# Kernel optimization log

Measured on AMD Instinct MI355X. Metric: run time of the kernel, lower is better.

The kernel has to match this reference:

```python
import jax, jax.numpy as jnp
import numpy as np
import math

N, E, G, D, H, L = 10000, 160000, 64, 480, 4, 6
DH = D // H          # 120 dims per head
NB = 128             # number of radial basis functions
SH = 9               # 1+3+5 spherical-harmonic channels (l=0,1,2)
CUTOFF = 5.0
AVG_DEG = 15.57930850982666
AVG_NODES = 18.03065905448718


def _silu(x):
    return x * jax.nn.sigmoid(x)


def _sph_harm(vec):
    # component-normalized real spherical harmonics l=0,1,2 on unit vectors
    r = jnp.linalg.norm(vec, axis=-1, keepdims=True) + 1e-12
    u = vec / r
    x, y, z = u[:, 0], u[:, 1], u[:, 2]
    s3, s5, s15 = math.sqrt(3.0), math.sqrt(5.0), math.sqrt(15.0)
    return jnp.stack([
        jnp.ones_like(x),
        s3 * x, s3 * y, s3 * z,
        s15 * x * y, s15 * y * z,
        0.5 * s5 * (3.0 * z * z - 1.0),
        s15 * x * z, 0.5 * s15 * (x * x - y * y)], axis=-1)


def _rbf(d):
    # Gaussian radial basis, centers on [0, cutoff]
    centers = jnp.linspace(0.0, CUTOFF, NB)
    width = CUTOFF / NB
    return jnp.exp(-jnp.square((d[:, None] - centers[None, :]) / width))


def _ln(x):
    mu = jnp.mean(x, axis=-1, keepdims=True)
    var = jnp.var(x, axis=-1, keepdims=True)
    return (x - mu) * jax.lax.rsqrt(var + 1e-5)


def setup_inputs() -> dict:
    key = jax.random.key(0)
    ks = jax.random.split(key, 24)

    def w(k, shape, fan_in):
        return jax.random.normal(k, shape, jnp.float32) / math.sqrt(fan_in)

    inp = {}
    inp["pos"] = jax.random.uniform(ks[0], (N, 3), jnp.float32) * 10.0
    inp["node_atom"] = jax.random.randint(ks[1], (N,), 0, 64)
    inp["edge_src"] = jax.random.randint(ks[2], (E,), 0, N)
    inp["edge_dst"] = jax.random.randint(ks[3], (E,), 0, N)
    inp["batch"] = jnp.sort(jax.random.randint(ks[4], (N,), 0, G))
    # learned parameters
    inp["atom_table"] = w(ks[5], (64, D), 1)
    inp["Wdeg"] = w(ks[6], (SH, D), SH)
    inp["Wd1"] = w(ks[7], (NB, 64), NB)
    inp["Wd2"] = w(ks[8], (64, 64), 64)
    inp["Wd3"] = w(ks[9], (64, 1), 64)
    inp["Wq"] = w(ks[10], (L, D, D), D)
    inp["Wk"] = w(ks[11], (L, D, D), D)
    inp["Wv"] = w(ks[12], (L, D, D), D)
    inp["Wsh"] = w(ks[13], (L, SH, D), SH)
    inp["W1"] = w(ks[14], (L, NB, 64), NB)
    inp["W2"] = w(ks[15], (L, 64, 64), 64)
    inp["W3"] = w(ks[16], (L, 64, H), 64)
    inp["Wo"] = w(ks[17], (L, D, D), D)
    inp["Wf1"] = w(ks[18], (L, D, 2 * D), D)
    inp["Wf2"] = w(ks[19], (L, 2 * D, D), 2 * D)
    inp["Wh1"] = w(ks[20], (D, D), D)
    inp["Wh2"] = w(ks[21], (D, 1), D)
    return inp


def reference(pos, atom_table, Wdeg, Wd1, Wd2, Wd3, Wq, Wk, Wv, Wsh, W1, W2, W3,
              Wo, Wf1, Wf2, Wh1, Wh2, node_atom, edge_src, edge_dst, batch):
    edge_vec = pos[edge_src] - pos[edge_dst]              # [E,3]
    sh = _sph_harm(edge_vec)                              # [E,SH]
    rbf = _rbf(jnp.linalg.norm(edge_vec, axis=-1))        # [E,NB]

    # atom embedding + edge-degree embedding (scatter-sum, rescaled)
    x = atom_table[node_atom]                             # [N,D]
    g0 = _silu(_silu(rbf @ Wd1) @ Wd2) @ Wd3              # [E,1]
    deg = jax.ops.segment_sum((sh @ Wdeg) * g0, edge_dst, num_segments=N)
    x = x + deg / math.sqrt(AVG_DEG)

    inv = 1.0 / math.sqrt(DH)
    for l in range(L):
        # per-edge q/k with SH tensor-product-style mixing and RBF gate
        q = (x @ Wq[l])[edge_dst].reshape(-1, H, DH)
        k = (x[edge_src] @ Wk[l] + sh @ Wsh[l]).reshape(-1, H, DH)
        gate = _silu(_silu(rbf @ W1[l]) @ W2[l]) @ W3[l]  # [E,H]
        logits = jnp.sum(q * k, axis=-1) * inv * gate      # [E,H]
        # per-neighborhood (destination node) softmax
        m = jax.ops.segment_max(logits, edge_dst, num_segments=N)
        a = jnp.exp(logits - m[edge_dst])
        den = jax.ops.segment_sum(a, edge_dst, num_segments=N)
        alpha = a / (den[edge_dst] + 1e-12)                # [E,H]
        v = (x @ Wv[l])[edge_src].reshape(-1, H, DH)
        msg = (alpha[..., None] * v).reshape(-1, D)
        agg = jax.ops.segment_sum(msg, edge_dst, num_segments=N)
        x = _ln(x + (agg / math.sqrt(AVG_DEG)) @ Wo[l])
        x = _ln(x + _silu(x @ Wf1[l]) @ Wf2[l])

    node_e = _silu(x @ Wh1) @ Wh2                          # [N,1]
    energy = jax.ops.segment_sum(node_e[:, 0], batch, num_segments=G) / AVG_NODES
    return energy
```

## Files before the change

### kernel.cpp

```cpp
#include <hip/hip_runtime.h>
#include <hip/hip_bf16.h>

#define NN 10000
#define EE 160000
#define GG 64
#define DD 480
#define HH 4
#define LLAYERS 6
#define DHD 120
#define NB_ 128
#define TSIZE 4096
#define DMAXT 5.5f
#define LSCALE (4095.0f/5.5f)

#define INV_DH 0.09128709291752768f
#define INV_SQRT_DEG 0.25335277f
#define INV_AVG_NODES (1.0f/18.03065905448718f)

typedef __attribute__((ext_vector_type(8))) short bf16x8;
typedef __attribute__((ext_vector_type(4))) float f32x4;
typedef __attribute__((ext_vector_type(8))) unsigned short u16x8;

__device__ __forceinline__ float b2f(unsigned short u){ return __uint_as_float(((unsigned)u)<<16); }
__device__ __forceinline__ unsigned short f2b(float f){
  unsigned u = __float_as_uint(f);
  return (unsigned short)((u + 0x7fffu + ((u>>16)&1u)) >> 16);
}
__device__ __forceinline__ float wsum(float v){
  #pragma unroll
  for (int off=32; off>0; off>>=1) v += __shfl_xor(v, off, 64);
  return v;
}
__device__ __forceinline__ void glds16(const void* g, void* l) {
  __builtin_amdgcn_global_load_lds((const __attribute__((address_space(1))) unsigned int*)g,
                                   (__attribute__((address_space(3))) unsigned int*)l, 16, 0, 0);
}

__global__ __launch_bounds__(256) void zero_kernel(int* __restrict__ cnt, float* __restrict__ out){
  int i = blockIdx.x*256 + threadIdx.x;
  if (i < NN) cnt[i] = 0;
  if (i < GG) out[i] = 0.f;
}

__global__ __launch_bounds__(256) void gather_x_kernel(const float* __restrict__ at,
    const int* __restrict__ atom, float* __restrict__ x){
  const int wid = threadIdx.x >> 6, lane = threadIdx.x & 63;
  for (int n = blockIdx.x*4 + wid; n < NN; n += gridDim.x*4) {
    int a = atom[n];
    if (lane < 60) {
      const float4* src = (const float4*)(at + (size_t)a*DD + lane*8);
      float4* dst = (float4*)(x + (size_t)n*DD + lane*8);
      dst[0] = src[0]; dst[1] = src[1];
    }
  }
}

__global__ __launch_bounds__(256) void edge_geom_kernel(const float* __restrict__ pos,
    const int* __restrict__ esrc, const int* __restrict__ edst,
    float* __restrict__ sh, float* __restrict__ dedge){
  const int e = blockIdx.x*256 + threadIdx.x;
  if (e >= EE) return;
  int s = esrc[e], d = edst[e];
  float vx = pos[s*3+0]-pos[d*3+0];
  float vy = pos[s*3+1]-pos[d*3+1];
  float vz = pos[s*3+2]-pos[d*3+2];
  float rr = sqrtf(vx*vx+vy*vy+vz*vz);
  dedge[e] = rr;
  float r = rr + 1e-12f;
  float x = vx/r, y = vy/r, z = vz/r;
  const float s3 = 1.7320508075688772f;
  const float s5 = 2.23606797749979f;
  const float s15 = 3.872983346207417f;
  float* o = sh + (size_t)e*9;
  o[0] = 1.f;
  o[1] = s3*x; o[2] = s3*y; o[3] = s3*z;
  o[4] = s15*x*y; o[5] = s15*y*z;
  o[6] = 0.5f*s5*(3.f*z*z-1.f);
  o[7] = s15*x*z;
  o[8] = 0.5f*s15*(x*x-y*y);
}

__global__ __launch_bounds__(256) void hist_kernel(const int* __restrict__ edst, int* __restrict__ cnt){
  int e = blockIdx.x*256 + threadIdx.x;
  if (e < EE) atomicAdd(&cnt[edst[e]], 1);
}

__global__ __launch_bounds__(1024) void scan_kernel(const int* __restrict__ cnt,
    int* __restrict__ row_ptr, int* __restrict__ cursor){
  __shared__ int sd[1024];
  __shared__ int s_carry;
  if (threadIdx.x == 0) s_carry = 0;
  __syncthreads();
  for (int base = 0; base < NN; base += 1024) {
    int i = base + threadIdx.x;
    int v = (i < NN) ? cnt[i] : 0;
    sd[threadIdx.x] = v;
    __syncthreads();
    for (int off = 1; off < 1024; off <<= 1) {
      int t = 0;
      if ((int)threadIdx.x >= off) t = sd[threadIdx.x - off];
      __syncthreads();
      sd[threadIdx.x] += t;
      __syncthreads();
    }
    int incl = sd[threadIdx.x];
    int carry = s_carry;
    if (i < NN) { row_ptr[i] = carry + incl - v; cursor[i] = carry + incl - v; }
    __syncthreads();
    if (threadIdx.x == 1023) s_carry = carry + incl;
    __syncthreads();
  }
  if (threadIdx.x == 0) row_ptr[NN] = s_carry;
}

__global__ __launch_bounds__(256) void scatter_kernel(const int* __restrict__ esrc,
    const int* __restrict__ edst, int* __restrict__ cursor,
    int* __restrict__ eid, int* __restrict__ srcs){
  int e = blockIdx.x*256 + threadIdx.x;
  if (e < EE) {
    int n = edst[e];
    int p = atomicAdd(&cursor[n], 1);
    eid[p] = e;
    srcs[p] = esrc[e];
  }
}

__global__ __launch_bounds__(256) void table_kernel(
    const float* __restrict__ Wd1, const float* __restrict__ Wd2, const float* __restrict__ Wd3,
    const float* __restrict__ W1, const float* __restrict__ W2, const float* __restrict__ W3,
    float* __restrict__ Tg, float* __restrict__ Tl) {
  const int chain = blockIdx.y;
  const float *A1, *A2, *A3; int NC;
  if (chain == 0) { A1 = Wd1; A2 = Wd2; A3 = Wd3; NC = 1; }
  else { int l = chain-1; A1 = W1 + (size_t)l*128*64; A2 = W2 + (size_t)l*64*64; A3 = W3 + (size_t)l*64*4; NC = 4; }
  __shared__ float W1s[128*64];
  __shared__ float W2s[64*64];
  __shared__ float W3s[64*4];
  for (int i = threadIdx.x; i < 128*64; i += 256) W1s[i] = A1[i];
  for (int i = threadIdx.x; i < 64*64; i += 256) W2s[i] = A2[i];
  for (int i = threadIdx.x; i < 64*4; i += 256) W3s[i] = (i < 64*NC) ? A3[i] : 0.f;
  __syncthreads();
  const int t = blockIdx.x*256 + threadIdx.x;
  const float d = (float)t * (DMAXT/(float)(TSIZE-1));
  float t1[64];
  #pragma unroll
  for (int c = 0; c < 64; ++c) t1[c] = 0.f;
  for (int j = 0; j < 128; ++j) {
    float z = (d - (float)j*(5.0f/127.0f)) * (128.0f/5.0f);
    float f = __expf(-z*z);
    #pragma unroll
    for (int c = 0; c < 64; ++c) t1[c] += f * W1s[j*64 + c];
  }
  #pragma unroll
  for (int c = 0; c < 64; ++c) t1[c] = t1[c] / (1.f + __expf(-t1[c]));
  float t2[64];
  #pragma unroll
  for (int c = 0; c < 64; ++c) t2[c] = 0.f;
  for (int c = 0; c < 64; ++c) {
    float v = t1[c];
    #pragma unroll
    for (int c2 = 0; c2 < 64; ++c2) t2[c2] += v * W2s[c*64 + c2];
  }
  #pragma unroll
  for (int c = 0; c < 64; ++c) t2[c] = t2[c] / (1.f + __expf(-t2[c]));
  if (chain == 0) {
    float o = 0.f;
    for (int c = 0; c < 64; ++c) o += t2[c] * W3s[c];
    Tg[t] = o;
  } else {
    #pragma unroll
    for (int nc = 0; nc < 4; ++nc) {
      float o = 0.f;
      for (int c = 0; c < 64; ++c) o += t2[c] * W3s[c*4 + nc];
      Tl[((size_t)(chain-1)*TSIZE + t)*4 + nc] = o;
    }
  }
}

__device__ __forceinline__ float lookup1(const float* __restrict__ Tg, float d) {
  float u = d * LSCALE;
  if (u >= (float)(TSIZE-1)) return 0.f;
  int i = (int)u; float fr = u - (float)i;
  float a = Tg[i], b = Tg[i+1];
  return a + fr*(b-a);
}

__global__ __launch_bounds__(256) void transpose_w_kernel(const float* __restrict__ W,
    __hip_bfloat16* __restrict__ Wt, int K, int N, int Npad,
    long long lstrideW, long long lstrideT) {
  __shared__ float T[32][33];
  const int l = blockIdx.z;
  W  += (size_t)l*lstrideW;
  Wt += (size_t)l*lstrideT;
  const int k0 = blockIdx.y*32, n0 = blockIdx.x*32;
  const int tx = threadIdx.x & 31, ty = threadIdx.x >> 5;
  #pragma unroll
  for (int r = 0; r < 32; r += 8) {
    int k = k0 + ty + r, n = n0 + tx;
    T[ty+r][tx] = (k < K && n < N) ? W[(size_t)k*N + n] : 0.f;
  }
  __syncthreads();
  #pragma unroll
  for (int r = 0; r < 32; r += 8) {
    int n = n0 + ty + r, k = k0 + tx;
    if (n < Npad && k < K)
      ((unsigned short*)Wt)[(size_t)n*K + k] = f2b(T[tx][ty+r]);
  }
}

template<int SILU, int OUT>
__global__ __launch_bounds__(256) void gemm_bf16_kernel(
    const __hip_bfloat16* __restrict__ A, const __hip_bfloat16* __restrict__ Bt,
    float* __restrict__ Cf, __hip_bfloat16* __restrict__ Cb0,
    __hip_bfloat16* __restrict__ Cb1, __hip_bfloat16* __restrict__ Cb2,
    int M, int K, int Nc) {
  __shared__ char smem[(512 + 256) * 16];
  char* AsB = smem;
  char* BsB = smem + 8192;
  const int tid = threadIdx.x;
  const int lane = tid & 63, wid = tid >> 6;
  const int wm = wid >> 1, wn = wid & 1;
  const long long m0 = (long long)blockIdx.y * 128;
  const int n0 = blockIdx.x * 64;

  const int arow_loc = (wid & 1)*64 + lane;
  long long gr = m0 + arow_loc; if (gr >= M) gr = M - 1;
  const __hip_bfloat16* aptr = A + gr * (size_t)K;
  const int khiA0 = wid >> 1, khiA1 = 2 + (wid >> 1);
  char* adst0 = AsB + wid*64*16;
  char* adst1 = AsB + 4096 + wid*64*16;
  const __hip_bfloat16* bptr = Bt + (size_t)(n0 + lane) * K;
  char* bdst = BsB + wid*64*16;

  f32x4 acc[4][2];
  #pragma unroll
  for (int i = 0; i < 4; ++i)
    #pragma unroll
    for (int j = 0; j < 2; ++j)
      acc[i][j] = (f32x4){0.f,0.f,0.f,0.f};

  const int lr = lane & 15, lkh = lane >> 4;

  for (int kt = 0; kt < K; kt += 32) {
    __syncthreads();
    glds16(aptr + kt + khiA0*8, adst0);
    glds16(aptr + kt + khiA1*8, adst1);
    glds16(bptr + kt + wid*8, bdst);
    __syncthreads();
    bf16x8 afr[4], bfr[2];
    #pragma unroll
    for (int fm = 0; fm < 4; ++fm)
      afr[fm] = *reinterpret_cast<const bf16x8*>(AsB + (lkh*128 + wm*64 + fm*16 + lr)*16);
    #pragma unroll
    for (int fn = 0; fn < 2; ++fn)
      bfr[fn] = *reinterpret_cast<const bf16x8*>(BsB + (lkh*64 + wn*32 + fn*16 + lr)*16);
    #pragma unroll
    for (int fm = 0; fm < 4; ++fm)
      #pragma unroll
      for (int fn = 0; fn < 2; ++fn)
        acc[fm][fn] = __builtin_amdgcn_mfma_f32_16x16x32_bf16(afr[fm], bfr[fn], acc[fm][fn], 0, 0, 0);
  }

  const int seg = n0 >> 9;
  const int c0 = (OUT == 2) ? (n0 & 511) : n0;
  unsigned short* qdst = nullptr;
  if (OUT == 2) qdst = (unsigned short*)(seg == 0 ? Cb0 : (seg == 1 ? Cb1 : Cb2));
  #pragma unroll
  for (int fm = 0; fm < 4; ++fm) {
    #pragma unroll
    for (int fn = 0; fn < 2; ++fn) {
      #pragma unroll
      for (int j = 0; j < 4; ++j) {
        long long r = m0 + wm*64 + fm*16 + lkh*4 + j;
        int c = c0 + wn*32 + fn*16 + lr;
        if (r < M && c < Nc) {
          float v = acc[fm][fn][j];
          if (SILU) v = v / (1.f + __expf(-v));
          if (OUT == 0) Cf[r*(size_t)Nc + c] = v;
          else if (OUT == 1) ((unsigned short*)Cb0)[r*(size_t)Nc + c] = f2b(v);
          else qdst[r*(size_t)Nc + c] = f2b(v);
        }
      }
    }
  }
}

__global__ __launch_bounds__(256) void deg_kernel(const float* __restrict__ dedge,
    const float* __restrict__ sh, const float* __restrict__ Tg,
    const int* __restrict__ row_ptr, const int* __restrict__ eid,
    const float* __restrict__ Wdeg, float* __restrict__ x, __hip_bfloat16* __restrict__ xb) {
  const int wid = threadIdx.x >> 6, lane = threadIdx.x & 63;
  for (int n = blockIdx.x*4 + wid; n < NN; n += gridDim.x*4) {
    const int e0 = row_ptr[n], e1 = row_ptr[n+1];
    float s9[9] = {0,0,0,0,0,0,0,0,0};
    for (int p = e0 + lane; p < e1; p += 64) {
      int e = eid[p];
      float g = lookup1(Tg, dedge[e]);
      const float* srow = sh + (size_t)e*9;
      #pragma unroll
      for (int s = 0; s < 9; ++s) s9[s] += g*srow[s];
    }
    #pragma unroll
    for (int s = 0; s < 9; ++s) s9[s] = wsum(s9[s]);
    #pragma unroll
    for (int r = 0; r < 8; ++r) {
      int d = lane + (r<<6);
      if (d < DD) {
        float acc = 0.f;
        #pragma unroll
        for (int s = 0; s < 9; ++s) acc += s9[s]*Wdeg[s*DD + d];
        float vv = x[(size_t)n*DD + d] + acc * INV_SQRT_DEG;
        x[(size_t)n*DD + d] = vv;
        ((unsigned short*)xb)[(size_t)n*DD + d] = f2b(vv);
      }
    }
  }
}

__global__ __launch_bounds__(256) void p_kernel(const __hip_bfloat16* __restrict__ xq,
    const float* __restrict__ Wsh_l, float* __restrict__ P) {
  const int wid = threadIdx.x >> 6, lane = threadIdx.x & 63;
  for (int n = blockIdx.x*4 + wid; n < NN; n += gridDim.x*4) {
    if (lane < 36) {
      int h = lane/9, s = lane%9;
      const unsigned short* q = (const unsigned short*)(xq + (size_t)n*DD + h*DHD);
      const float* w = Wsh_l + s*DD + h*DHD;
      float acc = 0.f;
      #pragma unroll
      for (int db = 0; db < 15; ++db) {
        u16x8 v = *reinterpret_cast<const u16x8*>(q + db*8);
        #pragma unroll
        for (int j = 0; j < 8; ++j) acc += b2f(v[j])*w[db*8+j];
      }
      P[(size_t)n*36 + lane] = acc;
    }
  }
}

__global__ __launch_bounds__(256) void coef_kernel(
    const int* __restrict__ eid, const int* __restrict__ edst,
    const float* __restrict__ sh, const float* __restrict__ dedge,
    const float* __restrict__ Tl, const float* __restrict__ P,
    float2* __restrict__ sb) {
  const int p = blockIdx.x*256 + threadIdx.x;
  if (p >= EE) return;
  const int e = eid[p];
  const int n = edst[e];
  const float* srow = sh + (size_t)e*9;
  float s0 = srow[0], s1 = srow[1], s2 = srow[2], s3 = srow[3], s4 = srow[4];
  float s5 = srow[5], s6 = srow[6], s7 = srow[7], s8 = srow[8];
  const float* Pn = P + (size_t)n*36;
  float g[4];
  {
    float u = dedge[e] * LSCALE;
    if (u >= (float)(TSIZE-1)) { g[0]=g[1]=g[2]=g[3]=0.f; }
    else {
      int ti = (int)u; float fr = u - (float)ti;
      const float4 ga = *reinterpret_cast<const float4*>(Tl + ti*4);
      const float4 gb = *reinterpret_cast<const float4*>(Tl + ti*4 + 4);
      g[0] = ga.x + fr*(gb.x-ga.x); g[1] = ga.y + fr*(gb.y-ga.y);
      g[2] = ga.z + fr*(gb.z-ga.z); g[3] = ga.w + fr*(gb.w-ga.w);
    }
  }
  #pragma unroll
  for (int h = 0; h < 4; ++h) {
    const float* Ph = Pn + h*9;
    float lp = s0*Ph[0]+s1*Ph[1]+s2*Ph[2]+s3*Ph[3]+s4*Ph[4]
             + s5*Ph[5]+s6*Ph[6]+s7*Ph[7]+s8*Ph[8];
    float sc = INV_DH * g[h];
    sb[(size_t)p*4 + h] = make_float2(sc, lp*sc);
  }
}

__global__ __launch_bounds__(256) void attn_kernel(
    const __hip_bfloat16* __restrict__ xq, const __hip_bfloat16* __restrict__ xk,
    const __hip_bfloat16* __restrict__ xv, const float2* __restrict__ sb,
    const int* __restrict__ row_ptr, const int* __restrict__ srcs,
    __hip_bfloat16* __restrict__ aggout) {
  const int wid = threadIdx.x >> 6, lane = threadIdx.x & 63;
  __shared__ float l_s[4][64][4];
  __shared__ int   src_sh[4][64];
  float (*ls)[4] = l_s[wid];
  int* srcS = src_sh[wid];
  const int hh = lane >> 4, li = lane & 15;
  const int hd = (lane < 60) ? (lane/15) : 3;
  const unsigned short* xkp = (const unsigned short*)xk;
  const unsigned short* xvp = (const unsigned short*)xv;
  const int doff = hh*DHD + li*8;
  for (int n = blockIdx.x*4 + wid; n < NN; n += gridDim.x*4) {
    const int e0 = row_ptr[n], e1 = row_ptr[n+1];
    float qf[8] = {0,0,0,0,0,0,0,0};
    if (li < 15) {
      u16x8 v = *reinterpret_cast<const u16x8*>((const unsigned short*)xq + (size_t)n*DD + doff);
      #pragma unroll
      for (int j = 0; j < 8; ++j) qf[j] = b2f(v[j]);
    }
    float m_reg = -1e30f, den_reg = 0.f;
    float agg[8] = {0,0,0,0,0,0,0,0};
    for (int c0 = e0; c0 < e1; c0 += 64) {
      const int cn = min(64, e1 - c0);
      if (lane < cn) srcS[lane] = srcs[c0 + lane];
      asm volatile("s_waitcnt lgkmcnt(0)" ::: "memory");
      int i = 0;
      for (; i + 4 <= cn; i += 4) {
        int sA = srcS[i], sB = srcS[i+1], sC = srcS[i+2], sD = srcS[i+3];
        float a0 = 0.f, a1 = 0.f, a2 = 0.f, a3 = 0.f;
        if (li < 15) {
          u16x8 k0 = *reinterpret_cast<const u16x8*>(xkp + (size_t)sA*DD + doff);
          u16x8 k1 = *reinterpret_cast<const u16x8*>(xkp + (size_t)sB*DD + doff);
          u16x8 k2 = *reinterpret_cast<const u16x8*>(xkp + (size_t)sC*DD + doff);
          u16x8 k3 = *reinterpret_cast<const u16x8*>(xkp + (size_t)sD*DD + doff);
          #pragma unroll
          for (int j = 0; j < 8; ++j) {
            a0 += qf[j]*b2f(k0[j]);
            a1 += qf[j]*b2f(k1[j]);
            a2 += qf[j]*b2f(k2[j]);
            a3 += qf[j]*b2f(k3[j]);
          }
        }
        #pragma unroll
        for (int off = 1; off < 16; off <<= 1) {
          a0 += __shfl_xor(a0, off, 64);
          a1 += __shfl_xor(a1, off, 64);
          a2 += __shfl_xor(a2, off, 64);
          a3 += __shfl_xor(a3, off, 64);
        }
        if (li == 0) {
          float2 cA = sb[(size_t)(c0+i+0)*4 + hh];
          float2 cB = sb[(size_t)(c0+i+1)*4 + hh];
          float2 cC = sb[(size_t)(c0+i+2)*4 + hh];
          float2 cD = sb[(size_t)(c0+i+3)*4 + hh];
          ls[i+0][hh] = a0*cA.x + cA.y;
          ls[i+1][hh] = a1*cB.x + cB.y;
          ls[i+2][hh] = a2*cC.x + cC.y;
          ls[i+3][hh] = a3*cD.x + cD.y;
        }
      }
      for (; i < cn; ++i) {
        int sA = srcS[i];
        float a0 = 0.f;
        if (li < 15) {
          u16x8 k0 = *reinterpret_cast<const u16x8*>(xkp + (size_t)sA*DD + doff);
          #pragma unroll
          for (int j = 0; j < 8; ++j) a0 += qf[j]*b2f(k0[j]);
        }
        #pragma unroll
        for (int off = 1; off < 16; off <<= 1) a0 += __shfl_xor(a0, off, 64);
        if (li == 0) {
          float2 cA = sb[(size_t)(c0+i)*4 + hh];
          ls[i][hh] = a0*cA.x + cA.y;
        }
      }
      asm volatile("s_waitcnt lgkmcnt(0)" ::: "memory");
      const int h = lane & 3, i0 = lane >> 2;
      float cm = -1e30f;
      for (int i2 = i0; i2 < cn; i2 += 16) cm = fmaxf(cm, ls[i2][h]);
      #pragma unroll
      for (int off = 4; off < 64; off <<= 1) cm = fmaxf(cm, __shfl_xor(cm, off, 64));
      const float newm = fmaxf(m_reg, cm);
      const float f = __expf(m_reg - newm);
      float cs = 0.f;
      for (int i2 = i0; i2 < cn; i2 += 16) {
        float a = __expf(ls[i2][h] - newm);
        ls[i2][h] = a;
        cs += a;
      }
      #pragma unroll
      for (int off = 4; off < 64; off <<= 1) cs += __shfl_xor(cs, off, 64);
      m_reg = newm;
      den_reg = den_reg*f + cs;
      asm volatile("s_waitcnt lgkmcnt(0)" ::: "memory");
      const float fh = __shfl(f, hd);
      #pragma unroll
      for (int j = 0; j < 8; ++j) agg[j] *= fh;
      i = 0;
      for (; i + 4 <= cn; i += 4) {
        int sA = srcS[i], sB = srcS[i+1], sC = srcS[i+2], sD = srcS[i+3];
        float a0 = ls[i][hd], a1 = ls[i+1][hd], a2 = ls[i+2][hd], a3 = ls[i+3][hd];
        if (lane < 60) {
          u16x8 v0 = *reinterpret_cast<const u16x8*>(xvp + (size_t)sA*DD + lane*8);
          u16x8 v1 = *reinterpret_cast<const u16x8*>(xvp + (size_t)sB*DD + lane*8);
          u16x8 v2 = *reinterpret_cast<const u16x8*>(xvp + (size_t)sC*DD + lane*8);
          u16x8 v3 = *reinterpret_cast<const u16x8*>(xvp + (size_t)sD*DD + lane*8);
          #pragma unroll
          for (int j = 0; j < 8; ++j)
            agg[j] += a0*b2f(v0[j]) + a1*b2f(v1[j]) + a2*b2f(v2[j]) + a3*b2f(v3[j]);
        }
      }
      for (; i < cn; ++i) {
        int sA = srcS[i];
        float a0 = ls[i][hd];
        if (lane < 60) {
          u16x8 v0 = *reinterpret_cast<const u16x8*>(xvp + (size_t)sA*DD + lane*8);
          #pragma unroll
          for (int j = 0; j < 8; ++j) agg[j] += a0*b2f(v0[j]);
        }
      }
    }
    const float dh2 = __shfl(den_reg, hd);
    if (lane < 60) {
      const float sc = INV_SQRT_DEG / (dh2 + 1e-12f);
      u16x8 o;
      #pragma unroll
      for (int j = 0; j < 8; ++j) o[j] = f2b(agg[j]*sc);
      *reinterpret_cast<u16x8*>((unsigned short*)aggout + (size_t)n*DD + lane*8) = o;
    }
  }
}

__global__ __launch_bounds__(256) void ln_kernel(float* __restrict__ x, const float* __restrict__ t,
    __hip_bfloat16* __restrict__ xb) {
  const int wid = threadIdx.x >> 6, lane = threadIdx.x & 63;
  for (int n = blockIdx.x*4 + wid; n < NN; n += gridDim.x*4) {
    float4 a0 = make_float4(0,0,0,0), a1 = make_float4(0,0,0,0);
    float s = 0.f, s2 = 0.f;
    if (lane < 60) {
      const float4* xp = (const float4*)(x + (size_t)n*DD + lane*8);
      const float4* tp = (const float4*)(t + (size_t)n*DD + lane*8);
      float4 b0 = tp[0], b1 = tp[1];
      a0 = xp[0]; a1 = xp[1];
      a0.x += b0.x; a0.y += b0.y; a0.z += b0.z; a0.w += b0.w;
      a1.x += b1.x; a1.y += b1.y; a1.z += b1.z; a1.w += b1.w;
      s  = a0.x+a0.y+a0.z+a0.w + a1.x+a1.y+a1.z+a1.w;
      s2 = a0.x*a0.x+a0.y*a0.y+a0.z*a0.z+a0.w*a0.w
         + a1.x*a1.x+a1.y*a1.y+a1.z*a1.z+a1.w*a1.w;
    }
    s = wsum(s); s2 = wsum(s2);
    const float mu = s * (1.f/(float)DD);
    const float var = s2 * (1.f/(float)DD) - mu*mu;
    const float rs = rsqrtf(var + 1e-5f);
    if (lane < 60) {
      float4* xp = (float4*)(x + (size_t)n*DD + lane*8);
      a0.x = (a0.x-mu)*rs; a0.y = (a0.y-mu)*rs; a0.z = (a0.z-mu)*rs; a0.w = (a0.w-mu)*rs;
      a1.x = (a1.x-mu)*rs; a1.y = (a1.y-mu)*rs; a1.z = (a1.z-mu)*rs; a1.w = (a1.w-mu)*rs;
      xp[0] = a0; xp[1] = a1;
      u16x8 o;
      o[0]=f2b(a0.x); o[1]=f2b(a0.y); o[2]=f2b(a0.z); o[3]=f2b(a0.w);
      o[4]=f2b(a1.x); o[5]=f2b(a1.y); o[6]=f2b(a1.z); o[7]=f2b(a1.w);
      *reinterpret_cast<u16x8*>((unsigned short*)xb + (size_t)n*DD + lane*8) = o;
    }
  }
}

__global__ __launch_bounds__(256) void h2_kernel(const float* __restrict__ t,
    const float* __restrict__ Wh2, const int* __restrict__ batch, float* __restrict__ out) {
  const int wid = threadIdx.x >> 6, lane = threadIdx.x & 63;
  for (int n = blockIdx.x*4 + wid; n < NN; n += gridDim.x*4) {
    float s = 0.f;
    if (lane < 60) {
      const float4* tp = (const float4*)(t + (size_t)n*DD + lane*8);
      const float4* wp = (const float4*)(Wh2 + lane*8);
      float4 t0 = tp[0], t1 = tp[1], w0 = wp[0], w1 = wp[1];
      s = t0.x*w0.x+t0.y*w0.y+t0.z*w0.z+t0.w*w0.w
        + t1.x*w1.x+t1.y*w1.y+t1.z*w1.z+t1.w*w1.w;
    }
    s = wsum(s);
    if (lane == 0) atomicAdd(&out[batch[n]], s * INV_AVG_NODES);
  }
}

extern "C" void kernel_launch(void* const* d_in, const int* in_sizes, int n_in,
                              void* d_out, int out_size, void* d_ws, size_t ws_size,
                              hipStream_t stream) {
  const float* pos        = (const float*)d_in[0];
  const int*   node_atom  = (const int*)  d_in[1];
  const int*   edge_src   = (const int*)  d_in[2];
  const int*   edge_dst   = (const int*)  d_in[3];
  const int*   batch      = (const int*)  d_in[4];
  const float* atom_table = (const float*)d_in[5];
  const float* Wdeg       = (const float*)d_in[6];
  const float* Wd1        = (const float*)d_in[7];
  const float* Wd2        = (const float*)d_in[8];
  const float* Wd3        = (const float*)d_in[9];
  const float* Wq         = (const float*)d_in[10];
  const float* Wk         = (const float*)d_in[11];
  const float* Wv         = (const float*)d_in[12];
  const float* Wsh        = (const float*)d_in[13];
  const float* W1         = (const float*)d_in[14];
  const float* W2         = (const float*)d_in[15];
  const float* W3         = (const float*)d_in[16];
  const float* Wo         = (const float*)d_in[17];
  const float* Wf1        = (const float*)d_in[18];
  const float* Wf2        = (const float*)d_in[19];
  const float* Wh1        = (const float*)d_in[20];
  const float* Wh2        = (const float*)d_in[21];
  float* out = (float*)d_out;
  char*  wsb = (char*)d_ws;

  size_t off = 0;
  auto alloc = [&](size_t bytes) { size_t o = off; off += (bytes + 255) & ~(size_t)255; return o; };
  float*  x      = (float*) (wsb + alloc((size_t)NN*DD*4));
  __hip_bfloat16* xb   = (__hip_bfloat16*)(wsb + alloc((size_t)NN*DD*2));
  __hip_bfloat16* xq   = (__hip_bfloat16*)(wsb + alloc((size_t)NN*DD*2));
  __hip_bfloat16* xk   = (__hip_bfloat16*)(wsb + alloc((size_t)NN*DD*2));
  __hip_bfloat16* xv   = (__hip_bfloat16*)(wsb + alloc((size_t)NN*DD*2));
  float*  shb    = (float*) (wsb + alloc((size_t)EE*9*4));
  float*  dedge  = (float*) (wsb + alloc((size_t)EE*4));
  float*  P      = (float*) (wsb + alloc((size_t)NN*36*4));
  float2* sbuf   = (float2*)(wsb + alloc((size_t)EE*4*8));
  __hip_bfloat16* aggb = (__hip_bfloat16*)(wsb + alloc((size_t)NN*DD*2));
  float*  tmp480 = (float*) (wsb + alloc((size_t)NN*DD*4));
  __hip_bfloat16* tmp960 = (__hip_bfloat16*)(wsb + alloc((size_t)NN*960*2));
  float*  Tg     = (float*) (wsb + alloc((size_t)TSIZE*4));
  float*  Tl     = (float*) (wsb + alloc((size_t)LLAYERS*TSIZE*4*4));
  __hip_bfloat16* Wqkvt = (__hip_bfloat16*)(wsb + alloc((size_t)LLAYERS*1536*480*2));
  __hip_bfloat16* Wot   = (__hip_bfloat16*)(wsb + alloc((size_t)LLAYERS*512*480*2));
  __hip_bfloat16* Wf1t  = (__hip_bfloat16*)(wsb + alloc((size_t)LLAYERS*960*480*2));
  __hip_bfloat16* Wf2t  = (__hip_bfloat16*)(wsb + alloc((size_t)LLAYERS*512*960*2));
  __hip_bfloat16* Wh1t  = (__hip_bfloat16*)(wsb + alloc((size_t)512*480*2));
  int* cnt     = (int*)(wsb + alloc((size_t)NN*4));
  int* row_ptr = (int*)(wsb + alloc((size_t)(NN+1)*4));
  int* cursor  = (int*)(wsb + alloc((size_t)NN*4));
  int* eid     = (int*)(wsb + alloc((size_t)EE*4));
  int* srcs    = (int*)(wsb + alloc((size_t)EE*4));
  (void)ws_size;

  auto tr = [&](const float* W, __hip_bfloat16* Wt, int K, int N, int Npad,
                long long lsW, long long lsT, int L) {
    dim3 g((Npad+31)/32, (K+31)/32, L);
    transpose_w_kernel<<<g, 256, 0, stream>>>(W, Wt, K, N, Npad, lsW, lsT);
  };

  tr(Wq,  Wqkvt + 0*512*480,    480, 480, 512, 480*480, 1536*480, LLAYERS);
  tr(Wk,  Wqkvt + 1*512*480,    480, 480, 512, 480*480, 1536*480, LLAYERS);
  tr(Wv,  Wqkvt + 2*512*480,    480, 480, 512, 480*480, 1536*480, LLAYERS);
  tr(Wo,  Wot,  480, 480, 512, 480*480, 512*480, LLAYERS);
  tr(Wf1, Wf1t, 480, 960, 960, 480*960, 960*480, LLAYERS);
  tr(Wf2, Wf2t, 960, 480, 512, 960*480, 512*960, LLAYERS);
  tr(Wh1, Wh1t, 480, 480, 512, 480*480, 512*480, 1);

  zero_kernel<<<(NN+255)/256, 256, 0, stream>>>(cnt, out);
  gather_x_kernel<<<640, 256, 0, stream>>>(atom_table, node_atom, x);
  edge_geom_kernel<<<(EE+255)/256, 256, 0, stream>>>(pos, edge_src, edge_dst, shb, dedge);
  hist_kernel<<<(EE+255)/256, 256, 0, stream>>>(edge_dst, cnt);
  scan_kernel<<<1, 1024, 0, stream>>>(cnt, row_ptr, cursor);
  scatter_kernel<<<(EE+255)/256, 256, 0, stream>>>(edge_src, edge_dst, cursor, eid, srcs);
  table_kernel<<<dim3(TSIZE/256, 1+LLAYERS), 256, 0, stream>>>(Wd1, Wd2, Wd3, W1, W2, W3, Tg, Tl);
  deg_kernel<<<2500, 256, 0, stream>>>(dedge, shb, Tg, row_ptr, eid, Wdeg, x, xb);

  for (int l = 0; l < LLAYERS; ++l) {
    const __hip_bfloat16* Wqkvt_l = Wqkvt + (size_t)l*1536*480;
    const __hip_bfloat16* Wot_l   = Wot   + (size_t)l*512*480;
    const __hip_bfloat16* Wf1t_l  = Wf1t  + (size_t)l*960*480;
    const __hip_bfloat16* Wf2t_l  = Wf2t  + (size_t)l*512*960;
    const float* Wsh_l = Wsh + (size_t)l*9*DD;
    const float* Tl_l  = Tl  + (size_t)l*TSIZE*4;

    gemm_bf16_kernel<0,2><<<dim3(24, 79), 256, 0, stream>>>(xb, Wqkvt_l, nullptr, xq, xk, xv, NN, 480, 480);
    p_kernel<<<2500, 256, 0, stream>>>(xq, Wsh_l, P);
    coef_kernel<<<(EE+255)/256, 256, 0, stream>>>(eid, edge_dst, shb, dedge, Tl_l, P, sbuf);
    attn_kernel<<<2500, 256, 0, stream>>>(xq, xk, xv, sbuf, row_ptr, srcs, aggb);
    gemm_bf16_kernel<0,0><<<dim3(8, 79), 256, 0, stream>>>(aggb, Wot_l, tmp480, nullptr, nullptr, nullptr, NN, 480, 480);
    ln_kernel<<<640, 256, 0, stream>>>(x, tmp480, xb);
    gemm_bf16_kernel<1,1><<<dim3(15, 79), 256, 0, stream>>>(xb, Wf1t_l, nullptr, tmp960, nullptr, nullptr, NN, 480, 960);
    gemm_bf16_kernel<0,0><<<dim3(8, 79), 256, 0, stream>>>(tmp960, Wf2t_l, tmp480, nullptr, nullptr, nullptr, NN, 960, 480);
    ln_kernel<<<640, 256, 0, stream>>>(x, tmp480, xb);
  }

  gemm_bf16_kernel<1,0><<<dim3(8, 79), 256, 0, stream>>>(xb, Wh1t, tmp480, nullptr, nullptr, nullptr, NN, 480, 480);
  h2_kernel<<<640, 256, 0, stream>>>(tmp480, Wh2, batch, out);
}
```

Measured before the change: 1.893 ms.

## Widen GEMM tiles, parallelize table MLP across lanes, pre-reduce energy per block

```diff
diff --git a/kernel.cpp b/kernel.cpp
--- a/kernel.cpp
+++ b/kernel.cpp
@@ -125,7 +125,7 @@
   }
 }
 
-__global__ __launch_bounds__(256) void table_kernel(
+__global__ __launch_bounds__(1024) void table_kernel(
     const float* __restrict__ Wd1, const float* __restrict__ Wd2, const float* __restrict__ Wd3,
     const float* __restrict__ W1, const float* __restrict__ W2, const float* __restrict__ W3,
     float* __restrict__ Tg, float* __restrict__ Tl) {
@@ -136,43 +136,36 @@
   __shared__ float W1s[128*64];
   __shared__ float W2s[64*64];
   __shared__ float W3s[64*4];
-  for (int i = threadIdx.x; i < 128*64; i += 256) W1s[i] = A1[i];
-  for (int i = threadIdx.x; i < 64*64; i += 256) W2s[i] = A2[i];
-  for (int i = threadIdx.x; i < 64*4; i += 256) W3s[i] = (i < 64*NC) ? A3[i] : 0.f;
+  for (int i = threadIdx.x; i < 128*64; i += 1024) W1s[i] = A1[i];
+  for (int i = threadIdx.x; i < 64*64; i += 1024) W2s[i] = A2[i];
+  for (int i = threadIdx.x; i < 64*4; i += 1024) W3s[i] = (i < 64*NC) ? A3[i] : 0.f;
   __syncthreads();
-  const int t = blockIdx.x*256 + threadIdx.x;
+  const int wid = threadIdx.x >> 6, lane = threadIdx.x & 63;
+  const int t = blockIdx.x*16 + wid;
   const float d = (float)t * (DMAXT/(float)(TSIZE-1));
-  float t1[64];
-  #pragma unroll
-  for (int c = 0; c < 64; ++c) t1[c] = 0.f;
+  float t1 = 0.f;
+  #pragma unroll 4
   for (int j = 0; j < 128; ++j) {
     float z = (d - (float)j*(5.0f/127.0f)) * (128.0f/5.0f);
     float f = __expf(-z*z);
-    #pragma unroll
-    for (int c = 0; c < 64; ++c) t1[c] += f * W1s[j*64 + c];
-  }
-  #pragma unroll
-  for (int c = 0; c < 64; ++c) t1[c] = t1[c] / (1.f + __expf(-t1[c]));
-  float t2[64];
-  #pragma unroll
-  for (int c = 0; c < 64; ++c) t2[c] = 0.f;
+    t1 += f * W1s[j*64 + lane];
+  }
+  t1 = t1 / (1.f + __expf(-t1));
+  float t2 = 0.f;
+  #pragma unroll 4
   for (int c = 0; c < 64; ++c) {
-    float v = t1[c];
-    #pragma unroll
-    for (int c2 = 0; c2 < 64; ++c2) t2[c2] += v * W2s[c*64 + c2];
-  }
-  #pragma unroll
-  for (int c = 0; c < 64; ++c) t2[c] = t2[c] / (1.f + __expf(-t2[c]));
+    float bc = __shfl(t1, c);
+    t2 += bc * W2s[c*64 + lane];
+  }
+  t2 = t2 / (1.f + __expf(-t2));
   if (chain == 0) {
-    float o = 0.f;
-    for (int c = 0; c < 64; ++c) o += t2[c] * W3s[c];
-    Tg[t] = o;
+    float o = wsum(t2 * W3s[lane]);
+    if (lane == 0) Tg[t] = o;
   } else {
     #pragma unroll
     for (int nc = 0; nc < 4; ++nc) {
-      float o = 0.f;
-      for (int c = 0; c < 64; ++c) o += t2[c] * W3s[c*4 + nc];
-      Tl[((size_t)(chain-1)*TSIZE + t)*4 + nc] = o;
+      float o = wsum(t2 * W3s[lane*4 + nc]);
+      if (lane == 0) Tl[((size_t)(chain-1)*TSIZE + t)*4 + nc] = o;
     }
   }
 }
@@ -209,28 +202,26 @@
 }
 
 template<int SILU, int OUT>
-__global__ __launch_bounds__(256) void gemm_bf16_kernel(
+__global__ __launch_bounds__(512) void gemm_bf16_kernel(
     const __hip_bfloat16* __restrict__ A, const __hip_bfloat16* __restrict__ Bt,
     float* __restrict__ Cf, __hip_bfloat16* __restrict__ Cb0,
     __hip_bfloat16* __restrict__ Cb1, __hip_bfloat16* __restrict__ Cb2,
     int M, int K, int Nc) {
-  __shared__ char smem[(512 + 256) * 16];
+  __shared__ char smem[16384];
   char* AsB = smem;
   char* BsB = smem + 8192;
   const int tid = threadIdx.x;
   const int lane = tid & 63, wid = tid >> 6;
-  const int wm = wid >> 1, wn = wid & 1;
+  const int wm = wid >> 2, wn = wid & 3;
   const long long m0 = (long long)blockIdx.y * 128;
-  const int n0 = blockIdx.x * 64;
-
-  const int arow_loc = (wid & 1)*64 + lane;
-  long long gr = m0 + arow_loc; if (gr >= M) gr = M - 1;
-  const __hip_bfloat16* aptr = A + gr * (size_t)K;
-  const int khiA0 = wid >> 1, khiA1 = 2 + (wid >> 1);
-  char* adst0 = AsB + wid*64*16;
-  char* adst1 = AsB + 4096 + wid*64*16;
-  const __hip_bfloat16* bptr = Bt + (size_t)(n0 + lane) * K;
-  char* bdst = BsB + wid*64*16;
+  const int n0 = blockIdx.x * 128;
+
+  const int skhi = wid >> 1, srow = (wid & 1)*64 + lane;
+  long long gra = m0 + srow; if (gra >= M) gra = M - 1;
+  const __hip_bfloat16* aptr = A + gra * (size_t)K + skhi*8;
+  const __hip_bfloat16* bptr = Bt + (size_t)(n0 + srow) * K + skhi*8;
+  char* adst = AsB + (skhi*128 + srow)*16;
+  char* bdst = BsB + (skhi*128 + srow)*16;
 
   f32x4 acc[4][2];
   #pragma unroll
@@ -243,9 +234,8 @@
 
   for (int kt = 0; kt < K; kt += 32) {
     __syncthreads();
-    glds16(aptr + kt + khiA0*8, adst0);
-    glds16(aptr + kt + khiA1*8, adst1);
-    glds16(bptr + kt + wid*8, bdst);
+    glds16(aptr + kt, adst);
+    glds16(bptr + kt, bdst);
     __syncthreads();
     bf16x8 afr[4], bfr[2];
     #pragma unroll
@@ -253,7 +243,7 @@
       afr[fm] = *reinterpret_cast<const bf16x8*>(AsB + (lkh*128 + wm*64 + fm*16 + lr)*16);
     #pragma unroll
     for (int fn = 0; fn < 2; ++fn)
-      bfr[fn] = *reinterpret_cast<const bf16x8*>(BsB + (lkh*64 + wn*32 + fn*16 + lr)*16);
+      bfr[fn] = *reinterpret_cast<const bf16x8*>(BsB + (lkh*128 + wn*32 + fn*16 + lr)*16);
     #pragma unroll
     for (int fm = 0; fm < 4; ++fm)
       #pragma unroll
@@ -544,8 +534,14 @@
 
 __global__ __launch_bounds__(256) void h2_kernel(const float* __restrict__ t,
     const float* __restrict__ Wh2, const int* __restrict__ batch, float* __restrict__ out) {
+  __shared__ float part[GG];
+  for (int i = threadIdx.x; i < GG; i += 256) part[i] = 0.f;
+  __syncthreads();
   const int wid = threadIdx.x >> 6, lane = threadIdx.x & 63;
-  for (int n = blockIdx.x*4 + wid; n < NN; n += gridDim.x*4) {
+  const int per_block = (NN + gridDim.x - 1) / gridDim.x;
+  const int n0 = blockIdx.x * per_block;
+  const int n1 = min(NN, n0 + per_block);
+  for (int n = n0 + wid; n < n1; n += 4) {
     float s = 0.f;
     if (lane < 60) {
       const float4* tp = (const float4*)(t + (size_t)n*DD + lane*8);
@@ -555,7 +551,12 @@
         + t1.x*w1.x+t1.y*w1.y+t1.z*w1.z+t1.w*w1.w;
     }
     s = wsum(s);
-    if (lane == 0) atomicAdd(&out[batch[n]], s * INV_AVG_NODES);
+    if (lane == 0) atomicAdd(&part[batch[n]], s * INV_AVG_NODES);
+  }
+  __syncthreads();
+  for (int i = threadIdx.x; i < GG; i += 256) {
+    float v = part[i];
+    if (v != 0.f) atomicAdd(&out[i], v);
   }
 }
 
@@ -605,7 +606,7 @@
   float*  Tl     = (float*) (wsb + alloc((size_t)LLAYERS*TSIZE*4*4));
   __hip_bfloat16* Wqkvt = (__hip_bfloat16*)(wsb + alloc((size_t)LLAYERS*1536*480*2));
   __hip_bfloat16* Wot   = (__hip_bfloat16*)(wsb + alloc((size_t)LLAYERS*512*480*2));
-  __hip_bfloat16* Wf1t  = (__hip_bfloat16*)(wsb + alloc((size_t)LLAYERS*960*480*2));
+  __hip_bfloat16* Wf1t  = (__hip_bfloat16*)(wsb + alloc((size_t)LLAYERS*1024*480*2));
   __hip_bfloat16* Wf2t  = (__hip_bfloat16*)(wsb + alloc((size_t)LLAYERS*512*960*2));
   __hip_bfloat16* Wh1t  = (__hip_bfloat16*)(wsb + alloc((size_t)512*480*2));
   int* cnt     = (int*)(wsb + alloc((size_t)NN*4));
@@ -625,7 +626,7 @@
   tr(Wk,  Wqkvt + 1*512*480,    480, 480, 512, 480*480, 1536*480, LLAYERS);
   tr(Wv,  Wqkvt + 2*512*480,    480, 480, 512, 480*480, 1536*480, LLAYERS);
   tr(Wo,  Wot,  480, 480, 512, 480*480, 512*480, LLAYERS);
-  tr(Wf1, Wf1t, 480, 960, 960, 480*960, 960*480, LLAYERS);
+  tr(Wf1, Wf1t, 480, 960, 1024, 480*960, 1024*480, LLAYERS);
   tr(Wf2, Wf2t, 960, 480, 512, 960*480, 512*960, LLAYERS);
   tr(Wh1, Wh1t, 480, 480, 512, 480*480, 512*480, 1);
 
@@ -635,28 +636,28 @@
   hist_kernel<<<(EE+255)/256, 256, 0, stream>>>(edge_dst, cnt);
   scan_kernel<<<1, 1024, 0, stream>>>(cnt, row_ptr, cursor);
   scatter_kernel<<<(EE+255)/256, 256, 0, stream>>>(edge_src, edge_dst, cursor, eid, srcs);
-  table_kernel<<<dim3(TSIZE/256, 1+LLAYERS), 256, 0, stream>>>(Wd1, Wd2, Wd3, W1, W2, W3, Tg, Tl);
+  table_kernel<<<dim3(TSIZE/16, 1+LLAYERS), 1024, 0, stream>>>(Wd1, Wd2, Wd3, W1, W2, W3, Tg, Tl);
   deg_kernel<<<2500, 256, 0, stream>>>(dedge, shb, Tg, row_ptr, eid, Wdeg, x, xb);
 
   for (int l = 0; l < LLAYERS; ++l) {
     const __hip_bfloat16* Wqkvt_l = Wqkvt + (size_t)l*1536*480;
     const __hip_bfloat16* Wot_l   = Wot   + (size_t)l*512*480;
-    const __hip_bfloat16* Wf1t_l  = Wf1t  + (size_t)l*960*480;
+    const __hip_bfloat16* Wf1t_l  = Wf1t  + (size_t)l*1024*480;
     const __hip_bfloat16* Wf2t_l  = Wf2t  + (size_t)l*512*960;
     const float* Wsh_l = Wsh + (size_t)l*9*DD;
     const float* Tl_l  = Tl  + (size_t)l*TSIZE*4;
 
-    gemm_bf16_kernel<0,2><<<dim3(24, 79), 256, 0, stream>>>(xb, Wqkvt_l, nullptr, xq, xk, xv, NN, 480, 480);
+    gemm_bf16_kernel<0,2><<<dim3(12, 79), 512, 0, stream>>>(xb, Wqkvt_l, nullptr, xq, xk, xv, NN, 480, 480);
     p_kernel<<<2500, 256, 0, stream>>>(xq, Wsh_l, P);
     coef_kernel<<<(EE+255)/256, 256, 0, stream>>>(eid, edge_dst, shb, dedge, Tl_l, P, sbuf);
     attn_kernel<<<2500, 256, 0, stream>>>(xq, xk, xv, sbuf, row_ptr, srcs, aggb);
-    gemm_bf16_kernel<0,0><<<dim3(8, 79), 256, 0, stream>>>(aggb, Wot_l, tmp480, nullptr, nullptr, nullptr, NN, 480, 480);
+    gemm_bf16_kernel<0,0><<<dim3(4, 79), 512, 0, stream>>>(aggb, Wot_l, tmp480, nullptr, nullptr, nullptr, NN, 480, 480);
     ln_kernel<<<640, 256, 0, stream>>>(x, tmp480, xb);
-    gemm_bf16_kernel<1,1><<<dim3(15, 79), 256, 0, stream>>>(xb, Wf1t_l, nullptr, tmp960, nullptr, nullptr, NN, 480, 960);
-    gemm_bf16_kernel<0,0><<<dim3(8, 79), 256, 0, stream>>>(tmp960, Wf2t_l, tmp480, nullptr, nullptr, nullptr, NN, 960, 480);
+    gemm_bf16_kernel<1,1><<<dim3(8, 79), 512, 0, stream>>>(xb, Wf1t_l, nullptr, tmp960, nullptr, nullptr, NN, 480, 960);
+    gemm_bf16_kernel<0,0><<<dim3(4, 79), 512, 0, stream>>>(tmp960, Wf2t_l, tmp480, nullptr, nullptr, nullptr, NN, 960, 480);
     ln_kernel<<<640, 256, 0, stream>>>(x, tmp480, xb);
   }
 
-  gemm_bf16_kernel<1,0><<<dim3(8, 79), 256, 0, stream>>>(xb, Wh1t, tmp480, nullptr, nullptr, nullptr, NN, 480, 480);
-  h2_kernel<<<640, 256, 0, stream>>>(tmp480, Wh2, batch, out);
-}
+  gemm_bf16_kernel<1,0><<<dim3(4, 79), 512, 0, stream>>>(xb, Wh1t, tmp480, nullptr, nullptr, nullptr, NN, 480, 480);
+  h2_kernel<<<160, 256, 0, stream>>>(tmp480, Wh2, batch, out);
+}
```

Result: faster. 1.734 ms (-8.4%).
